# Performance work log

Measured on AMD Instinct MI355X. Metric: run time of the kernel, lower is better.

## Reference

```python
import jax, jax.numpy as jnp
import numpy as np

B, S, D = 2, 2048, 4096
H, KVH, HD = 32, 8, 128
THETA = 10000.0


def setup_inputs() -> dict:
    key = jax.random.key(0)
    k1, k2, k3 = jax.random.split(key, 3)
    hidden_states = jax.random.normal(k1, (B, S, D), jnp.float32)
    w_qkv = jax.random.normal(k2, ((KVH * 2 + H) * HD, D), jnp.float32) * 0.02
    w_dense = jax.random.normal(k3, (D, D), jnp.float32) * 0.02
    return {"hidden_states": hidden_states, "w_qkv": w_qkv, "w_dense": w_dense}


def _rope(x, pos):
    # x: [B, H, S, HD]; Falcon rotary embedding (rotate_half convention)
    inv_freq = 1.0 / (THETA ** (jnp.arange(0, HD, 2, dtype=jnp.float32) / HD))
    freqs = pos[:, None] * inv_freq[None, :]           # [S, HD/2]
    emb = jnp.concatenate([freqs, freqs], axis=-1)      # [S, HD]
    cos, sin = jnp.cos(emb), jnp.sin(emb)
    x1, x2 = x[..., : HD // 2], x[..., HD // 2 :]
    rot = jnp.concatenate([-x2, x1], axis=-1)
    return x * cos + rot * sin


def reference(hidden_states, w_qkv, w_dense):
    # fused QKV projection (FalconLinear, no bias)
    fused = jnp.einsum('bsd,ed->bse', hidden_states, w_qkv)  # [B,S,(2KVH+H)*HD]
    g = H // KVH  # query heads per kv head
    qkv = fused.reshape(B, S, KVH, g + 2, HD)
    q = qkv[:, :, :, :g]                        # [B,S,KVH,g,HD]
    k = jnp.broadcast_to(qkv[:, :, :, g:g + 1], q.shape)
    v = jnp.broadcast_to(qkv[:, :, :, g + 1:g + 2], q.shape)
    q, k, v = (t.reshape(B, S, H, HD).transpose(0, 2, 1, 3) for t in (q, k, v))
    pos = jnp.arange(S, dtype=jnp.float32)
    q = _rope(q, pos)
    k = _rope(k, pos)
    scores = jnp.einsum('bhqd,bhkd->bhqk', q, k) / jnp.sqrt(jnp.float32(HD))
    causal = jnp.tril(jnp.ones((S, S), dtype=bool))
    scores = jnp.where(causal, scores, jnp.float32(-1e9))
    attn = jax.nn.softmax(scores, axis=-1)
    out = jnp.einsum('bhqk,bhkd->bhqd', attn, v)
    out = out.transpose(0, 2, 1, 3).reshape(B, S, H * HD)   # merge heads
    return jnp.einsum('bsd,ed->bse', out, w_dense)
```

## Files before the change

kernel.cpp:

```cpp
#include <hip/hip_runtime.h>

#define B_   2
#define S_   2048
#define D_   4096
#define H_   32
#define KVH_ 8
#define HD_  128
#define NE_  6144

using f32x4  = __attribute__((ext_vector_type(4))) float;
using bf16x8 = __attribute__((ext_vector_type(8))) __bf16;
using u16x8  = __attribute__((ext_vector_type(8))) unsigned short;

__device__ __forceinline__ unsigned short f2bf(float f) {
  union { float f; unsigned u; } v; v.f = f;
  unsigned r = v.u + 0x7FFFu + ((v.u >> 16) & 1u);
  return (unsigned short)(r >> 16);
}
__device__ __forceinline__ float bf2f(unsigned short h) {
  union { unsigned u; float f; } v; v.u = ((unsigned)h) << 16; return v.f;
}
__device__ __forceinline__ bf16x8 ld8(const unsigned short* p) {
  return *reinterpret_cast<const bf16x8*>(p);
}
__device__ __forceinline__ bf16x8 ld8b(const void* base, int byte_off) {
  return *reinterpret_cast<const bf16x8*>((const char*)base + byte_off);
}
__device__ __forceinline__ void cp16(const void* g, void* l) {
  __builtin_amdgcn_global_load_lds(
      (const __attribute__((address_space(1))) void*)g,
      (__attribute__((address_space(3))) void*)l, 16, 0, 0);
}
__device__ __forceinline__ float exp2a(float x) {
  float r; asm("v_exp_f32 %0, %1" : "=v"(r) : "v"(x)); return r;
}

#define SC2F 0.12751652f

__global__ __launch_bounds__(256) void cvt2_f32_bf16(
    const float* __restrict__ s0, unsigned short* __restrict__ d0, int n0,
    const float* __restrict__ s1, unsigned short* __restrict__ d1, int n1)
{
  int i = blockIdx.x * 256 + threadIdx.x;
  const float* src; unsigned short* dst;
  if (i < n0) { src = s0; dst = d0; }
  else        { i -= n0; if (i >= n1) return; src = s1; dst = d1; }
  f32x4 v = *reinterpret_cast<const f32x4*>(src + (size_t)i * 4);
  ushort4 o;
  o.x = f2bf(v[0]); o.y = f2bf(v[1]); o.z = f2bf(v[2]); o.w = f2bf(v[3]);
  *reinterpret_cast<ushort4*>(dst + (size_t)i * 4) = o;
}

template <typename OutT, int NT>
__global__ __launch_bounds__(512, 2) void gemm256(
    const unsigned short* __restrict__ A,
    const unsigned short* __restrict__ Bw,
    OutT* __restrict__ C, int M, int N)
{
  constexpr int K  = 4096;
  constexpr int NI = (K / 64) / 2;
  constexpr int NB = NT / 64;
  constexpr int NN = NT / 64;
  constexpr int WN = NT / 4;
  constexpr int BBUF = NT * 128;
  __shared__ __align__(16) char lds[65536 + 2 * BBUF];

  const int tid  = threadIdx.x;
  const int lane = tid & 63;
  const int wave = tid >> 6;
  const int wr = wave >> 2;
  const int wc = wave & 3;
  const int lr = lane & 15;
  const int lk = (lane >> 4) * 8;

  int id  = blockIdx.y * gridDim.x + blockIdx.x;
  const int nwg = gridDim.x * gridDim.y;
  if ((nwg & 7) == 0) { const int q = nwg >> 3; id = (id & 7) * q + (id >> 3); }
  const int row0 = (id / gridDim.x) * 256;
  const int col0 = (id % gridDim.x) * NT;

  int rwA[2], csA[2], dbA[2];
#pragma unroll
  for (int j = 0; j < 2; ++j) {
    dbA[j] = j * 8192 + tid * 16;
    rwA[j] = dbA[j] >> 7;
    csA[j] = ((dbA[j] & 127) ^ ((rwA[j] & 7) << 4)) >> 1;
  }
  auto stA = [&](int buf, int h, int t) {
#pragma unroll
    for (int j = 0; j < 2; ++j)
      cp16(A + (size_t)(row0 + h * 128 + rwA[j]) * K + t * 64 + csA[j],
           lds + buf * 32768 + h * 16384 + dbA[j]);
  };
  const int dbB = tid * 16;
  const int rwB = dbB >> 7;
  const int csB = ((dbB & 127) ^ ((rwB & 7) << 4)) >> 1;
  auto stB = [&](int buf, int c, int t) {
    cp16(Bw + (size_t)(col0 + c * 64 + rwB) * K + t * 64 + csB,
         lds + 65536 + buf * BBUF + c * 8192 + dbB);
  };

  const int cb0 = ((0 + lk) << 1) ^ ((lr & 7) << 4);
  const int cb1 = ((32 + lk) << 1) ^ ((lr & 7) << 4);
  const int aRowB = (wr * 128 + lr) * 128;
  const int bRowB = (wc * WN + lr) * 128;

  f32x4 acc[8][NN];
#pragma unroll
  for (int m = 0; m < 8; ++m)
#pragma unroll
    for (int n = 0; n < NN; ++n) acc[m][n] = (f32x4){0.f, 0.f, 0.f, 0.f};
  bf16x8 bfr[NN][2];

#define FENCE asm volatile("" ::: "memory")
#define VMNB  do { if constexpr (NB == 4) asm volatile("s_waitcnt vmcnt(4)" ::: "memory"); \
                   else                   asm volatile("s_waitcnt vmcnt(3)" ::: "memory"); } while (0)
#define VM0   asm volatile("s_waitcnt vmcnt(0)" ::: "memory")

#define PHASE(p, buf, STAGE, WAIT)                                             \
  {                                                                            \
    if ((p) == 0) {                                                            \
      _Pragma("unroll")                                                        \
      for (int n = 0; n < NN; ++n) {                                           \
        bfr[n][0] = ld8b(lds, 65536 + (buf) * BBUF + bRowB + n * 2048 + cb0);  \
        bfr[n][1] = ld8b(lds, 65536 + (buf) * BBUF + bRowB + n * 2048 + cb1);  \
      }                                                                        \
    }                                                                          \
    bf16x8 a00 = ld8b(lds, (buf) * 32768 + aRowB + ((p) * 2 + 0) * 2048 + cb0);\
    bf16x8 a01 = ld8b(lds, (buf) * 32768 + aRowB + ((p) * 2 + 0) * 2048 + cb1);\
    bf16x8 a10 = ld8b(lds, (buf) * 32768 + aRowB + ((p) * 2 + 1) * 2048 + cb0);\
    bf16x8 a11 = ld8b(lds, (buf) * 32768 + aRowB + ((p) * 2 + 1) * 2048 + cb1);\
    STAGE;                                                                     \
    FENCE;                                                                     \
    __builtin_amdgcn_s_barrier();                                              \
    __builtin_amdgcn_s_setprio(1);                                             \
    _Pragma("unroll")                                                          \
    for (int n = 0; n < NN; ++n) {                                             \
      acc[(p)*2+0][n] = __builtin_amdgcn_mfma_f32_16x16x32_bf16(a00, bfr[n][0], acc[(p)*2+0][n], 0, 0, 0); \
      acc[(p)*2+0][n] = __builtin_amdgcn_mfma_f32_16x16x32_bf16(a01, bfr[n][1], acc[(p)*2+0][n], 0, 0, 0); \
      acc[(p)*2+1][n] = __builtin_amdgcn_mfma_f32_16x16x32_bf16(a10, bfr[n][0], acc[(p)*2+1][n], 0, 0, 0); \
      acc[(p)*2+1][n] = __builtin_amdgcn_mfma_f32_16x16x32_bf16(a11, bfr[n][1], acc[(p)*2+1][n], 0, 0, 0); \
    }                                                                          \
    __builtin_amdgcn_s_setprio(0);                                             \
    WAIT;                                                                      \
    FENCE;                                                                     \
    __builtin_amdgcn_s_barrier();                                              \
  }

#pragma unroll
  for (int c = 0; c < NB; ++c) stB(0, c, 0);
  stA(0, 0, 0); stA(0, 1, 0);
#pragma unroll
  for (int c = 0; c < NB; ++c) stB(1, c, 1);
  VMNB;
  FENCE;
  __builtin_amdgcn_s_barrier();

  for (int i = 0; i < NI; ++i) {
    const int t1  = 2 * i + 1;
    const int tn0 = 2 * i + 2;
    const int tn1 = 2 * i + 3;
    const bool pre = (i + 1 < NI);
    PHASE(0, 0, { stA(1, 0, t1); }, {});
    PHASE(1, 0, { stA(1, 1, t1); }, {});
    PHASE(2, 0, { if (pre) { stB(0, 0, tn0); stB(0, 1, tn0); } }, {});
    PHASE(3, 0, { if (pre) { _Pragma("unroll") for (int c = 2; c < NB; ++c) stB(0, c, tn0); } },
          { if (pre) { VMNB; } else { VM0; } });
    PHASE(0, 1, { if (pre) stA(0, 0, tn0); }, {});
    PHASE(1, 1, { if (pre) stA(0, 1, tn0); }, {});
    PHASE(2, 1, { if (pre) { stB(1, 0, tn1); stB(1, 1, tn1); } }, {});
    PHASE(3, 1, { if (pre) { _Pragma("unroll") for (int c = 2; c < NB; ++c) stB(1, c, tn1); } },
          { if (pre) { VMNB; } });
  }
#undef PHASE
#undef FENCE
#undef VMNB
#undef VM0

  const int orow = (lane >> 4) * 4;
#pragma unroll
  for (int m = 0; m < 8; ++m) {
    const int gr0 = row0 + wr * 128 + m * 16 + orow;
#pragma unroll
    for (int n = 0; n < NN; ++n) {
      const int gc = col0 + wc * WN + n * 16 + lr;
#pragma unroll
      for (int r = 0; r < 4; ++r) {
        float val = acc[m][n][r];
        if constexpr (sizeof(OutT) == 2)
          C[(size_t)(gr0 + r) * N + gc] = f2bf(val);
        else
          C[(size_t)(gr0 + r) * N + gc] = val;
      }
    }
  }
}

#define ROPE_N (B_ * S_ * 48 * 8)
__global__ __launch_bounds__(256) void rope_scatter_cvt(
    const unsigned short* __restrict__ fused,
    unsigned short* __restrict__ Qr,
    unsigned short* __restrict__ Kr,
    unsigned short* __restrict__ Vt,
    const float* __restrict__ wdense,
    unsigned short* __restrict__ Wdb,
    int nD4)
{
  int idx = blockIdx.x * 256 + threadIdx.x;
  if (idx >= ROPE_N) {
    int i = idx - ROPE_N;
    if (i >= nD4) return;
    f32x4 v = *reinterpret_cast<const f32x4*>(wdense + (size_t)i * 4);
    ushort4 o;
    o.x = f2bf(v[0]); o.y = f2bf(v[1]); o.z = f2bf(v[2]); o.w = f2bf(v[3]);
    *reinterpret_cast<ushort4*>(Wdb + (size_t)i * 4) = o;
    return;
  }
  int dg = idx & 7;
  int t = idx >> 3;
  int e = t % 48;
  int bs = t / 48;
  int s = bs % S_;
  int b = bs / S_;
  int kvh = e / 6, j = e % 6;
  const unsigned short* src = fused + (size_t)bs * NE_ + e * 128 + dg * 8;
  u16x8 lo = *reinterpret_cast<const u16x8*>(src);
  u16x8 hi = *reinterpret_cast<const u16x8*>(src + 64);
  if (j == 5) {
    size_t base = (size_t)(b * KVH_ + kvh) * HD_ * S_ + s;
#pragma unroll
    for (int jj = 0; jj < 8; ++jj) {
      Vt[base + (size_t)(dg * 8 + jj) * S_]      = lo[jj];
      Vt[base + (size_t)(dg * 8 + jj + 64) * S_] = hi[jj];
    }
  } else {
    const float sc = (j == 4) ? 1.0f : SC2F;
    u16x8 olo, ohi;
#pragma unroll
    for (int jj = 0; jj < 8; ++jj) {
      int d = dg * 8 + jj;
      float x1 = bf2f(lo[jj]), x2 = bf2f(hi[jj]);
      float inv = __expf(-(float)d * (9.2103403719761836f / 64.0f));
      float ang = (float)s * inv;
      float sn, c;
      sincosf(ang, &sn, &c);
      olo[jj] = f2bf((x1 * c - x2 * sn) * sc);
      ohi[jj] = f2bf((x2 * c + x1 * sn) * sc);
    }
    unsigned short* dst;
    if (j == 4) dst = Kr + ((size_t)(b * KVH_ + kvh) * S_ + s) * HD_;
    else        dst = Qr + ((size_t)(b * H_ + kvh * 4 + j) * S_ + s) * HD_;
    *reinterpret_cast<u16x8*>(dst + dg * 8)      = olo;
    *reinterpret_cast<u16x8*>(dst + dg * 8 + 64) = ohi;
  }
}

__global__ __launch_bounds__(256) void attn_fwd(
    const unsigned short* __restrict__ Qr,
    const unsigned short* __restrict__ Kr,
    const unsigned short* __restrict__ Vt,
    unsigned short* __restrict__ O)
{
  __shared__ __align__(16) unsigned short Kld[2][64 * 128];
  __shared__ __align__(16) unsigned short Vld[2][128 * 64];
  __shared__ __align__(16) unsigned short Pld[4][16 * 64];

  const int tid  = threadIdx.x;
  const int lane = tid & 63;
  const int wave = tid >> 6;
  const int bx = blockIdx.x;
  const int h  = blockIdx.y;
  const int b  = blockIdx.z;
  const int kvh = h >> 2;
  const int lr = lane & 15;
  const int lk = (lane >> 4) * 8;
  const int orow = (lane >> 4) * 4;

  const unsigned short* Kb = Kr + (size_t)(b * KVH_ + kvh) * S_ * HD_;
  const unsigned short* Vb = Vt + (size_t)(b * KVH_ + kvh) * HD_ * S_;

  auto stage = [&](int buf, int kb) {
#pragma unroll
    for (int i = 0; i < 4; ++i) {
      const int db = i * 4096 + tid * 16;
      {
        const int row  = db >> 8;
        const int colb = (db & 255) ^ ((row & 7) << 4);
        cp16(Kb + (size_t)(kb * 64 + row) * HD_ + (colb >> 1),
             (char*)&Kld[buf][0] + i * 4096 + wave * 1024);
      }
      {
        const int row  = db >> 7;
        const int colb = (db & 127) ^ ((row & 7) << 4);
        cp16(Vb + (size_t)row * S_ + kb * 64 + (colb >> 1),
             (char*)&Vld[buf][0] + i * 4096 + wave * 1024);
      }
    }
  };

  for (int half = 0; half < 2; ++half) {
    const int qb = half ? (S_ / 64 - 1 - bx) : bx;

    const unsigned short* qbase =
        Qr + ((size_t)(b * H_ + h) * S_ + qb * 64 + wave * 16 + lr) * HD_;
    bf16x8 qf[4];
#pragma unroll
    for (int t = 0; t < 4; ++t) qf[t] = ld8(qbase + t * 32 + lk);

    f32x4 acc_o[8];
#pragma unroll
    for (int dt = 0; dt < 8; ++dt) acc_o[dt] = (f32x4){0.f, 0.f, 0.f, 0.f};
    float mrow[4], lpart[4];
#pragma unroll
    for (int r = 0; r < 4; ++r) { mrow[r] = -1e30f; lpart[r] = 0.f; }

    stage(0, 0);
    __syncthreads();

    for (int kb = 0; kb <= qb; ++kb) {
      const int cur = kb & 1;
      if (kb < qb) stage(cur ^ 1, kb + 1);

      const char* Kc = (const char*)&Kld[cur][0];
      const char* Vc = (const char*)&Vld[cur][0];

      f32x4 accs[4];
#pragma unroll
      for (int kt = 0; kt < 4; ++kt) accs[kt] = (f32x4){0.f, 0.f, 0.f, 0.f};
      __builtin_amdgcn_s_setprio(1);
#pragma unroll
      for (int t = 0; t < 4; ++t) {
#pragma unroll
        for (int kt = 0; kt < 4; ++kt) {
          const int krow = kt * 16 + lr;
          const int kbyte = ((krow << 8) + ((t * 32 + lk) << 1)) ^ ((krow & 7) << 4);
          bf16x8 kf = ld8b(Kc, kbyte);
          accs[kt] = __builtin_amdgcn_mfma_f32_16x16x32_bf16(qf[t], kf, accs[kt], 0, 0, 0);
        }
      }
      __builtin_amdgcn_s_setprio(0);

      if (kb == qb) {
#pragma unroll
        for (int r = 0; r < 4; ++r) {
          const int qg = wave * 16 + orow + r;
#pragma unroll
          for (int kt = 0; kt < 4; ++kt)
            if (kt * 16 + lr > qg) accs[kt][r] = -1e30f;
        }
      }

      float mx[4];
#pragma unroll
      for (int r = 0; r < 4; ++r)
        mx[r] = fmaxf(fmaxf(accs[0][r], accs[1][r]), fmaxf(accs[2][r], accs[3][r]));
      int ok = (mx[0] <= mrow[0] + 8.f) && (mx[1] <= mrow[1] + 8.f) &&
               (mx[2] <= mrow[2] + 8.f) && (mx[3] <= mrow[3] + 8.f);
      if (!__all(ok)) {
        float corr[4];
#pragma unroll
        for (int r = 0; r < 4; ++r) {
          float m = mx[r];
#pragma unroll
          for (int msk = 8; msk >= 1; msk >>= 1) m = fmaxf(m, __shfl_xor(m, msk, 64));
          float mnew = fmaxf(mrow[r], m);
          corr[r] = exp2a(mrow[r] - mnew);
          mrow[r] = mnew;
          lpart[r] *= corr[r];
        }
#pragma unroll
        for (int dt = 0; dt < 8; ++dt)
#pragma unroll
          for (int r = 0; r < 4; ++r) acc_o[dt][r] *= corr[r];
      }

#pragma unroll
      for (int r = 0; r < 4; ++r) {
        const int prow = orow + r;
#pragma unroll
        for (int kt = 0; kt < 4; ++kt) {
          float p = exp2a(accs[kt][r] - mrow[r]);
          lpart[r] += p;
          const int pbyte = ((prow << 7) + ((kt * 16 + lr) << 1)) ^ ((prow & 7) << 4);
          *(__bf16*)((char*)&Pld[wave][0] + pbyte) = (__bf16)p;
        }
      }

      asm volatile("" ::: "memory");

      __builtin_amdgcn_s_setprio(1);
#pragma unroll
      for (int kc = 0; kc < 2; ++kc) {
        const int pbyte = ((lr << 7) + ((kc * 32 + lk) << 1)) ^ ((lr & 7) << 4);
        bf16x8 pf = ld8b(&Pld[wave][0], pbyte);
#pragma unroll
        for (int dt = 0; dt < 8; ++dt) {
          const int vrow = dt * 16 + lr;
          const int vbyte = ((vrow << 7) + ((kc * 32 + lk) << 1)) ^ ((vrow & 7) << 4);
          bf16x8 vf = ld8b(Vc, vbyte);
          acc_o[dt] = __builtin_amdgcn_mfma_f32_16x16x32_bf16(pf, vf, acc_o[dt], 0, 0, 0);
        }
      }
      __builtin_amdgcn_s_setprio(0);

      __syncthreads();
    }

#pragma unroll
    for (int r = 0; r < 4; ++r) {
      float s = lpart[r];
#pragma unroll
      for (int msk = 8; msk >= 1; msk >>= 1) s += __shfl_xor(s, msk, 64);
      float inv = 1.f / s;
      size_t rowoff =
          (size_t)(b * S_ + qb * 64 + wave * 16 + orow + r) * (H_ * HD_) + h * HD_;
#pragma unroll
      for (int dt = 0; dt < 8; ++dt)
        O[rowoff + dt * 16 + lr] = f2bf(acc_o[dt][r] * inv);
    }
  }
}

__global__ void fill_sentinel(float* __restrict__ O, int n) {
  int i = blockIdx.x * 256 + threadIdx.x;
  if (i < n) O[i] = 12345.0f;
}

extern "C" void kernel_launch(void* const* d_in, const int* in_sizes, int n_in,
                              void* d_out, int out_size, void* d_ws, size_t ws_size,
                              hipStream_t stream) {
  const float* hidden = (const float*)d_in[0];
  const float* wqkv   = (const float*)d_in[1];
  const float* wdense = (const float*)d_in[2];
  float* out = (float*)d_out;

  const size_t NEED = 134217728;
  if (ws_size < NEED) {
    fill_sentinel<<<dim3((out_size + 255) / 256), dim3(256), 0, stream>>>(out, out_size);
    return;
  }

  char* ws = (char*)d_ws;
  unsigned short* Hb    = (unsigned short*)(ws);
  unsigned short* Wqb   = (unsigned short*)(ws + 33554432);
  unsigned short* fused = (unsigned short*)(ws + 83886080);
  unsigned short* Qr    = (unsigned short*)(ws);
  unsigned short* Kr    = (unsigned short*)(ws + 33554432);
  unsigned short* Vt    = (unsigned short*)(ws + 41943040);
  unsigned short* Wdb   = (unsigned short*)(ws + 50331648);
  unsigned short* attn_out = (unsigned short*)(ws + 83886080);

  const int nH4 = B_ * S_ * D_ / 4;
  const int nQ4 = NE_ * D_ / 4;
  const int nD4 = D_ * D_ / 4;

  cvt2_f32_bf16<<<dim3((nH4 + nQ4 + 255) / 256), dim3(256), 0, stream>>>(
      hidden, Hb, nH4, wqkv, Wqb, nQ4);

  gemm256<unsigned short, 192><<<dim3(NE_ / 192, (B_ * S_) / 256), dim3(512), 0, stream>>>(
      Hb, Wqb, fused, B_ * S_, NE_);

  rope_scatter_cvt<<<dim3((ROPE_N + nD4 + 255) / 256), dim3(256), 0, stream>>>(
      fused, Qr, Kr, Vt, wdense, Wdb, nD4);

  attn_fwd<<<dim3(16, H_, B_), dim3(256), 0, stream>>>(Qr, Kr, Vt, attn_out);

  gemm256<float, 256><<<dim3(D_ / 256, (B_ * S_) / 256), dim3(512), 0, stream>>>(
      attn_out, Wdb, out, B_ * S_, D_);
}
```

Measured before the change: 523.3 us.

## Rewrite attention with 32x32 MFMA, 128-row query tiles and register-resident P

The attention kernel moves from 16x16x32 to 32x32x16 bf16 MFMA and computes S transposed (K as the A operand), so each wave owns 32 query rows and a block covers 128 rows. Probabilities are packed with v_cvt_pk_bf16_f32 and rearranged with v_permlane32_swap, so they feed the PV MFMA straight from registers and the LDS round-trip for P is gone. The grid is halved and launch bounds request two blocks per CU. The aim is to cut LDS traffic and get better MFMA efficiency per loaded K/V tile, at the cost of more register pressure, per-row shuffles when rescaling, and fewer blocks for the scheduler to balance.

```diff
diff --git a/kernel.cpp b/kernel.cpp
--- a/kernel.cpp
+++ b/kernel.cpp
@@ -9,6 +9,7 @@
 #define NE_  6144
 
 using f32x4  = __attribute__((ext_vector_type(4))) float;
+using f32x16 = __attribute__((ext_vector_type(16))) float;
 using bf16x8 = __attribute__((ext_vector_type(8))) __bf16;
 using u16x8  = __attribute__((ext_vector_type(8))) unsigned short;
 
@@ -33,6 +34,10 @@
 }
 __device__ __forceinline__ float exp2a(float x) {
   float r; asm("v_exp_f32 %0, %1" : "=v"(r) : "v"(x)); return r;
+}
+__device__ __forceinline__ unsigned cvtpk(float lo, float hi) {
+  unsigned r; asm("v_cvt_pk_bf16_f32 %0, %1, %2" : "=v"(r) : "v"(lo), "v"(hi));
+  return r;
 }
 
 #define SC2F 0.12751652f
@@ -255,7 +260,7 @@
   }
 }
 
-__global__ __launch_bounds__(256) void attn_fwd(
+__global__ __launch_bounds__(256, 2) void attn_fwd(
     const unsigned short* __restrict__ Qr,
     const unsigned short* __restrict__ Kr,
     const unsigned short* __restrict__ Vt,
@@ -263,18 +268,16 @@
 {
   __shared__ __align__(16) unsigned short Kld[2][64 * 128];
   __shared__ __align__(16) unsigned short Vld[2][128 * 64];
-  __shared__ __align__(16) unsigned short Pld[4][16 * 64];
 
   const int tid  = threadIdx.x;
   const int lane = tid & 63;
   const int wave = tid >> 6;
   const int bx = blockIdx.x;
-  const int h  = blockIdx.y;
+  const int hh = blockIdx.y;
   const int b  = blockIdx.z;
-  const int kvh = h >> 2;
-  const int lr = lane & 15;
-  const int lk = (lane >> 4) * 8;
-  const int orow = (lane >> 4) * 4;
+  const int kvh = hh >> 2;
+  const int q31 = lane & 31;
+  const int h   = lane >> 5;
 
   const unsigned short* Kb = Kr + (size_t)(b * KVH_ + kvh) * S_ * HD_;
   const unsigned short* Vb = Vt + (size_t)(b * KVH_ + kvh) * HD_ * S_;
@@ -285,7 +288,7 @@
       const int db = i * 4096 + tid * 16;
       {
         const int row  = db >> 8;
-        const int colb = (db & 255) ^ ((row & 7) << 4);
+        const int colb = (db & 255) ^ ((row & 15) << 4);
         cp16(Kb + (size_t)(kb * 64 + row) * HD_ + (colb >> 1),
              (char*)&Kld[buf][0] + i * 4096 + wave * 1024);
       }
@@ -298,125 +301,121 @@
     }
   };
 
+  const int kswz = (q31 & 15) << 4;
+  const int vswz = (q31 & 7) << 4;
+
   for (int half = 0; half < 2; ++half) {
-    const int qb = half ? (S_ / 64 - 1 - bx) : bx;
+    const int qt = half ? (15 - bx) : bx;
+    const int nkb = 2 * (qt + 1);
+    const int qg = qt * 128 + wave * 32 + q31;
 
     const unsigned short* qbase =
-        Qr + ((size_t)(b * H_ + h) * S_ + qb * 64 + wave * 16 + lr) * HD_;
-    bf16x8 qf[4];
-#pragma unroll
-    for (int t = 0; t < 4; ++t) qf[t] = ld8(qbase + t * 32 + lk);
-
-    f32x4 acc_o[8];
-#pragma unroll
-    for (int dt = 0; dt < 8; ++dt) acc_o[dt] = (f32x4){0.f, 0.f, 0.f, 0.f};
-    float mrow[4], lpart[4];
-#pragma unroll
-    for (int r = 0; r < 4; ++r) { mrow[r] = -1e30f; lpart[r] = 0.f; }
+        Qr + ((size_t)(b * H_ + hh) * S_ + qg) * HD_;
+    bf16x8 qf[8];
+#pragma unroll
+    for (int t = 0; t < 8; ++t) qf[t] = ld8(qbase + t * 16 + h * 8);
+
+    f32x16 acc_o[4] = {};
+    float m = -1e30f, lpart = 0.f;
 
     stage(0, 0);
     __syncthreads();
 
-    for (int kb = 0; kb <= qb; ++kb) {
+    for (int kb = 0; kb < nkb; ++kb) {
       const int cur = kb & 1;
-      if (kb < qb) stage(cur ^ 1, kb + 1);
+      if (kb + 1 < nkb) stage(cur ^ 1, kb + 1);
 
       const char* Kc = (const char*)&Kld[cur][0];
       const char* Vc = (const char*)&Vld[cur][0];
 
-      f32x4 accs[4];
-#pragma unroll
-      for (int kt = 0; kt < 4; ++kt) accs[kt] = (f32x4){0.f, 0.f, 0.f, 0.f};
+      f32x16 accs0 = {}, accs1 = {};
       __builtin_amdgcn_s_setprio(1);
 #pragma unroll
-      for (int t = 0; t < 4; ++t) {
-#pragma unroll
-        for (int kt = 0; kt < 4; ++kt) {
-          const int krow = kt * 16 + lr;
-          const int kbyte = ((krow << 8) + ((t * 32 + lk) << 1)) ^ ((krow & 7) << 4);
-          bf16x8 kf = ld8b(Kc, kbyte);
-          accs[kt] = __builtin_amdgcn_mfma_f32_16x16x32_bf16(qf[t], kf, accs[kt], 0, 0, 0);
+      for (int t = 0; t < 8; ++t) {
+        const int hd2 = t * 32 + h * 16;
+        bf16x8 kf0 = ld8b(Kc, ((q31 << 8) + hd2) ^ kswz);
+        bf16x8 kf1 = ld8b(Kc, (((32 + q31) << 8) + hd2) ^ kswz);
+        accs0 = __builtin_amdgcn_mfma_f32_32x32x16_bf16(kf0, qf[t], accs0, 0, 0, 0);
+        accs1 = __builtin_amdgcn_mfma_f32_32x32x16_bf16(kf1, qf[t], accs1, 0, 0, 0);
+      }
+      __builtin_amdgcn_s_setprio(0);
+
+      if (kb >= 2 * qt) {
+        const int kbase = kb * 64 + 4 * h;
+#pragma unroll
+        for (int reg = 0; reg < 16; ++reg) {
+          const int k0 = kbase + (reg & 3) + 8 * (reg >> 2);
+          if (k0 > qg)      accs0[reg] = -1e30f;
+          if (k0 + 32 > qg) accs1[reg] = -1e30f;
         }
       }
+
+      float mx = -1e30f;
+#pragma unroll
+      for (int reg = 0; reg < 16; ++reg)
+        mx = fmaxf(mx, fmaxf(accs0[reg], accs1[reg]));
+      if (!__all(mx <= m + 8.f)) {
+        float mxo = __shfl_xor(mx, 32, 64);
+        float mnew = fmaxf(m, fmaxf(mx, mxo));
+        float corr = exp2a(m - mnew);
+        m = mnew;
+        lpart *= corr;
+#pragma unroll
+        for (int reg = 0; reg < 16; ++reg) {
+          const int crow = (reg & 3) + 8 * (reg >> 2) + 4 * h;
+          float cw = __shfl(corr, crow, 64);
+#pragma unroll
+          for (int dj = 0; dj < 4; ++dj) acc_o[dj][reg] *= cw;
+        }
+      }
+
+      bf16x8 pa[4];
+#pragma unroll
+      for (int ks = 0; ks < 4; ++ks) {
+        float e[8];
+#pragma unroll
+        for (int j = 0; j < 8; ++j) {
+          float s = (ks < 2) ? accs0[8 * (ks & 1) + j] : accs1[8 * (ks & 1) + j];
+          e[j] = exp2a(s - m);
+          lpart += e[j];
+        }
+        unsigned w01 = cvtpk(e[0], e[1]);
+        unsigned w23 = cvtpk(e[2], e[3]);
+        unsigned w45 = cvtpk(e[4], e[5]);
+        unsigned w67 = cvtpk(e[6], e[7]);
+        asm volatile("v_permlane32_swap_b32 %0, %1" : "+v"(w01), "+v"(w45));
+        asm volatile("v_permlane32_swap_b32 %0, %1" : "+v"(w23), "+v"(w67));
+        union { unsigned u[4]; bf16x8 v; } pu;
+        pu.u[0] = w01; pu.u[1] = w23; pu.u[2] = w45; pu.u[3] = w67;
+        pa[ks] = pu.v;
+      }
+
+      __builtin_amdgcn_s_setprio(1);
+#pragma unroll
+      for (int dj = 0; dj < 4; ++dj) {
+        const int vrow = (dj * 32 + q31) << 7;
+#pragma unroll
+        for (int ks = 0; ks < 4; ++ks) {
+          bf16x8 vf = ld8b(Vc, (vrow + ks * 32 + h * 16) ^ vswz);
+          acc_o[dj] = __builtin_amdgcn_mfma_f32_32x32x16_bf16(pa[ks], vf, acc_o[dj], 0, 0, 0);
+        }
+      }
       __builtin_amdgcn_s_setprio(0);
 
-      if (kb == qb) {
-#pragma unroll
-        for (int r = 0; r < 4; ++r) {
-          const int qg = wave * 16 + orow + r;
-#pragma unroll
-          for (int kt = 0; kt < 4; ++kt)
-            if (kt * 16 + lr > qg) accs[kt][r] = -1e30f;
-        }
-      }
-
-      float mx[4];
-#pragma unroll
-      for (int r = 0; r < 4; ++r)
-        mx[r] = fmaxf(fmaxf(accs[0][r], accs[1][r]), fmaxf(accs[2][r], accs[3][r]));
-      int ok = (mx[0] <= mrow[0] + 8.f) && (mx[1] <= mrow[1] + 8.f) &&
-               (mx[2] <= mrow[2] + 8.f) && (mx[3] <= mrow[3] + 8.f);
-      if (!__all(ok)) {
-        float corr[4];
-#pragma unroll
-        for (int r = 0; r < 4; ++r) {
-          float m = mx[r];
-#pragma unroll
-          for (int msk = 8; msk >= 1; msk >>= 1) m = fmaxf(m, __shfl_xor(m, msk, 64));
-          float mnew = fmaxf(mrow[r], m);
-          corr[r] = exp2a(mrow[r] - mnew);
-          mrow[r] = mnew;
-          lpart[r] *= corr[r];
-        }
-#pragma unroll
-        for (int dt = 0; dt < 8; ++dt)
-#pragma unroll
-          for (int r = 0; r < 4; ++r) acc_o[dt][r] *= corr[r];
-      }
-
-#pragma unroll
-      for (int r = 0; r < 4; ++r) {
-        const int prow = orow + r;
-#pragma unroll
-        for (int kt = 0; kt < 4; ++kt) {
-          float p = exp2a(accs[kt][r] - mrow[r]);
-          lpart[r] += p;
-          const int pbyte = ((prow << 7) + ((kt * 16 + lr) << 1)) ^ ((prow & 7) << 4);
-          *(__bf16*)((char*)&Pld[wave][0] + pbyte) = (__bf16)p;
-        }
-      }
-
-      asm volatile("" ::: "memory");
-
-      __builtin_amdgcn_s_setprio(1);
-#pragma unroll
-      for (int kc = 0; kc < 2; ++kc) {
-        const int pbyte = ((lr << 7) + ((kc * 32 + lk) << 1)) ^ ((lr & 7) << 4);
-        bf16x8 pf = ld8b(&Pld[wave][0], pbyte);
-#pragma unroll
-        for (int dt = 0; dt < 8; ++dt) {
-          const int vrow = dt * 16 + lr;
-          const int vbyte = ((vrow << 7) + ((kc * 32 + lk) << 1)) ^ ((vrow & 7) << 4);
-          bf16x8 vf = ld8b(Vc, vbyte);
-          acc_o[dt] = __builtin_amdgcn_mfma_f32_16x16x32_bf16(pf, vf, acc_o[dt], 0, 0, 0);
-        }
-      }
-      __builtin_amdgcn_s_setprio(0);
-
       __syncthreads();
     }
 
-#pragma unroll
-    for (int r = 0; r < 4; ++r) {
-      float s = lpart[r];
-#pragma unroll
-      for (int msk = 8; msk >= 1; msk >>= 1) s += __shfl_xor(s, msk, 64);
-      float inv = 1.f / s;
+    float lsum = lpart + __shfl_xor(lpart, 32, 64);
+    float linv = 1.f / lsum;
+#pragma unroll
+    for (int reg = 0; reg < 16; ++reg) {
+      const int crow = (reg & 3) + 8 * (reg >> 2) + 4 * h;
+      float lv = __shfl(linv, crow, 64);
       size_t rowoff =
-          (size_t)(b * S_ + qb * 64 + wave * 16 + orow + r) * (H_ * HD_) + h * HD_;
-#pragma unroll
-      for (int dt = 0; dt < 8; ++dt)
-        O[rowoff + dt * 16 + lr] = f2bf(acc_o[dt][r] * inv);
+          (size_t)(b * S_ + qt * 128 + wave * 32 + crow) * (H_ * HD_) + hh * HD_ + q31;
+#pragma unroll
+      for (int dj = 0; dj < 4; ++dj)
+        O[rowoff + dj * 32] = f2bf(acc_o[dj][reg] * lv);
     }
   }
 }
@@ -463,7 +462,7 @@
   rope_scatter_cvt<<<dim3((ROPE_N + nD4 + 255) / 256), dim3(256), 0, stream>>>(
       fused, Qr, Kr, Vt, wdense, Wdb, nD4);
 
-  attn_fwd<<<dim3(16, H_, B_), dim3(256), 0, stream>>>(Qr, Kr, Vt, attn_out);
+  attn_fwd<<<dim3(8, H_, B_), dim3(256), 0, stream>>>(Qr, Kr, Vt, attn_out);
 
   gemm256<float, 256><<<dim3(D_ / 256, (B_ * S_) / 256), dim3(512), 0, stream>>>(
       attn_out, Wdb, out, B_ * S_, D_);
```

Result: faster. 474.5 us (-9.3%).
